# Kernel optimization log

Measured on AMD Instinct MI355X. Metric: run time of the kernel, lower is better.

Reference implementation:

```python
import jax, jax.numpy as jnp
import numpy as np

DIM = 2048
H = 16
HKV = 4
D = DIM // H          # 128 head_dim
ROPE_BASE = 10000.0
TRAIN_SEQ_LEN = 1024
EPS = float(np.finfo(np.float32).eps)  # torch F.rms_norm default eps


def setup_inputs() -> dict:
    key = jax.random.key(0)
    ks = jax.random.split(key, 6)
    B, T = 2, 2048
    return {
        "x": jax.random.normal(ks[0], (B, T, DIM), jnp.float32),
        "q_w": jax.random.normal(ks[1], (DIM, DIM), jnp.float32) * 0.02,
        "k_w": jax.random.normal(ks[2], (HKV * D, DIM), jnp.float32) * 0.02,
        "v_w": jax.random.normal(ks[3], (HKV * D, DIM), jnp.float32) * 0.02,
        "out_w": jax.random.normal(ks[4], (DIM, DIM), jnp.float32) * 0.02,
        "q_gain": jnp.ones((H,), jnp.float32),
    }


def _rope_tables(T, dtype):
    rd = D  # rope_dims == head_dim (rope_dims=0 in module)
    if T > TRAIN_SEQ_LEN:
        scale = T / TRAIN_SEQ_LEN
        base = ROPE_BASE * scale ** (rd / (rd - 2))
    else:
        base = ROPE_BASE
    inv_freq = 1.0 / base ** (np.arange(0, rd, 2, dtype=np.float32) / rd)
    t = np.arange(T, dtype=np.float32)
    freqs = np.outer(t, inv_freq)  # [T, rd/2]
    cos = jnp.asarray(np.cos(freqs), dtype)[None, :, None, :]  # [1,T,1,rd/2]
    sin = jnp.asarray(np.sin(freqs), dtype)[None, :, None, :]
    return cos, sin


def _rms_norm(x):
    var = jnp.mean(jnp.square(x), axis=-1, keepdims=True)
    return x * jax.lax.rsqrt(var + EPS)


def _apply_rotary(x, cos, sin):
    half = x.shape[-1] // 2
    x1, x2 = x[..., :half], x[..., half:]
    return jnp.concatenate((x1 * cos + x2 * sin, -x1 * sin + x2 * cos), axis=-1)


def reference(x, q_w, k_w, v_w, out_w, q_gain):
    B, T, dim = x.shape
    q = (x @ q_w.T).reshape(B, T, H, D)
    k = (x @ k_w.T).reshape(B, T, HKV, D)
    v = (x @ v_w.T).reshape(B, T, HKV, D)
    q = _rms_norm(q)
    k = _rms_norm(k)
    cos, sin = _rope_tables(T, q.dtype)
    q = _apply_rotary(q, cos, sin)
    k = _apply_rotary(k, cos, sin)
    q = q * q_gain[None, None, :, None]
    rep = H // HKV
    k_r = jnp.repeat(k, rep, axis=2)  # [B,T,H,D]
    v_r = jnp.repeat(v, rep, axis=2)
    scores = jnp.einsum('bqhd,bkhd->bhqk', q, k_r) / jnp.sqrt(jnp.asarray(D, q.dtype))
    causal = jnp.tril(jnp.ones((T, T), bool))
    scores = jnp.where(causal[None, None], scores, jnp.asarray(-jnp.inf, scores.dtype))
    p = jax.nn.softmax(scores, axis=-1)
    y = jnp.einsum('bhqk,bkhd->bqhd', p, v_r).reshape(B, T, dim)
    return y @ out_w.T
```

## Files before the change

kernel.cpp:

```cpp
#include <hip/hip_runtime.h>
#include <hip/hip_bf16.h>

typedef __bf16 bf16x8 __attribute__((ext_vector_type(8)));
typedef unsigned short u16x8 __attribute__((ext_vector_type(8)));
typedef float f32x4 __attribute__((ext_vector_type(4)));
typedef __hip_bfloat16 bf16;

#define GLOAD_LDS16(g, l)                                               \
  __builtin_amdgcn_global_load_lds(                                     \
      (__attribute__((address_space(1))) void*)(void*)(g),              \
      (__attribute__((address_space(3))) void*)(void*)(l), 16, 0, 0)

__global__ __launch_bounds__(256) void cvt_all(
    const float4* __restrict__ x,  const float4* __restrict__ qw,
    const float4* __restrict__ kw, const float4* __restrict__ vw,
    const float4* __restrict__ ow,
    ushort4* __restrict__ xb,  ushort4* __restrict__ qwb,
    ushort4* __restrict__ kwb, ushort4* __restrict__ vwb,
    ushort4* __restrict__ owb)
{
  const int i = blockIdx.x * 256 + threadIdx.x;
  const float4* s; ushort4* d; int off;
  if      (i < 2097152) { s = x;  d = xb;  off = i; }
  else if (i < 3145728) { s = qw; d = qwb; off = i - 2097152; }
  else if (i < 3407872) { s = kw; d = kwb; off = i - 3145728; }
  else if (i < 3670016) { s = vw; d = vwb; off = i - 3407872; }
  else                  { s = ow; d = owb; off = i - 3670016; }
  float4 v = s[off];
  bf16 b0 = __float2bfloat16(v.x), b1 = __float2bfloat16(v.y);
  bf16 b2 = __float2bfloat16(v.z), b3 = __float2bfloat16(v.w);
  ushort4 o;
  o.x = *(unsigned short*)&b0; o.y = *(unsigned short*)&b1;
  o.z = *(unsigned short*)&b2; o.w = *(unsigned short*)&b3;
  d[off] = o;
}

__device__ __forceinline__ void store_out(bf16* p, float v)  { *p = __float2bfloat16(v); }
__device__ __forceinline__ void store_out(float* p, float v) { *p = v; }

template <typename OutT>
__device__ __forceinline__ void gemm_tile_body(
    const bf16* __restrict__ A, const bf16* __restrict__ W, OutT* __restrict__ C,
    int bm, int bn, int N, int K, bf16* As, bf16* Ws)
{
  const int tid  = threadIdx.x;
  const int lane = tid & 63;
  const int wave = tid >> 6;
  const int wm = (wave >> 1) * 64;
  const int wn = (wave & 1) * 64;
  const int mfrag = lane & 15;
  const int kfrag = (lane >> 4) * 8;

  f32x4 acc[4][4] = {};

  for (int k0 = 0; k0 < K; k0 += 32) {
#pragma unroll
    for (int r = 0; r < 2; ++r) {
      const int off  = r * 4096 + wave * 1024 + lane * 16;
      const int row  = off >> 6;
      const int colb = off & 63;
      const char* ga = (const char*)A + ((size_t)(bm + row) * K + k0) * 2 + colb;
      GLOAD_LDS16(ga, (char*)As + r * 4096 + wave * 1024);
      const char* gw = (const char*)W + ((size_t)(bn + row) * K + k0) * 2 + colb;
      GLOAD_LDS16(gw, (char*)Ws + r * 4096 + wave * 1024);
    }
    __syncthreads();

    bf16x8 af[4], wf[4];
#pragma unroll
    for (int i = 0; i < 4; ++i)
      af[i] = *(const bf16x8*)(As + (wm + i * 16 + mfrag) * 32 + kfrag);
#pragma unroll
    for (int j = 0; j < 4; ++j)
      wf[j] = *(const bf16x8*)(Ws + (wn + j * 16 + mfrag) * 32 + kfrag);
#pragma unroll
    for (int i = 0; i < 4; ++i)
#pragma unroll
      for (int j = 0; j < 4; ++j)
        acc[i][j] = __builtin_amdgcn_mfma_f32_16x16x32_bf16(af[i], wf[j], acc[i][j], 0, 0, 0);
    __syncthreads();
  }

  const int rq = (lane >> 4) * 4;
#pragma unroll
  for (int i = 0; i < 4; ++i)
#pragma unroll
    for (int j = 0; j < 4; ++j)
#pragma unroll
      for (int r = 0; r < 4; ++r) {
        const int row = bm + wm + i * 16 + rq + r;
        const int col = bn + wn + j * 16 + mfrag;
        store_out(&C[(size_t)row * N + col], acc[i][j][r]);
      }
}

__global__ __launch_bounds__(256) void gemm_bt_f32out(
    const bf16* __restrict__ A, const bf16* __restrict__ W, float* __restrict__ C,
    int N, int K)
{
  __shared__ bf16 As[128 * 32];
  __shared__ bf16 Ws[128 * 32];
  gemm_tile_body<float>(A, W, C, blockIdx.y * 128, blockIdx.x * 128, N, K, As, Ws);
}

__global__ __launch_bounds__(256) void gemm_qkv(
    const bf16* __restrict__ X, const bf16* __restrict__ Wq,
    const bf16* __restrict__ Wk, const bf16* __restrict__ Wv,
    bf16* __restrict__ Qo, bf16* __restrict__ Ko, bf16* __restrict__ Vo, int K)
{
  __shared__ bf16 As[128 * 32];
  __shared__ bf16 Ws[128 * 32];
  const int bx = blockIdx.x;
  const bf16* W; bf16* C; int N, bn;
  if (bx < 16)      { W = Wq; C = Qo; N = 2048; bn = bx * 128; }
  else if (bx < 20) { W = Wk; C = Ko; N = 512;  bn = (bx - 16) * 128; }
  else              { W = Wv; C = Vo; N = 512;  bn = (bx - 20) * 128; }
  gemm_tile_body<bf16>(X, W, C, blockIdx.y * 128, bn, N, K, As, Ws);
}

__device__ __forceinline__ void rope_row(
    bf16* __restrict__ buf, const float* __restrict__ gain,
    int nh, float scale, int row)
{
  const int j = threadIdx.x & 63;
  const int bt = row / nh;
  const int h  = row - bt * nh;
  const int t  = bt & 2047;
  bf16* p = buf + (size_t)bt * (nh * 128) + h * 128;

  float x1 = __bfloat162float(p[j]);
  float x2 = __bfloat162float(p[j + 64]);
  float ss = x1 * x1 + x2 * x2;
#pragma unroll
  for (int off = 32; off > 0; off >>= 1) ss += __shfl_xor(ss, off, 64);
  const float rinv = rsqrtf(ss * (1.0f / 128.0f) + 1.1920928955078125e-07f);
  const float g = gain ? gain[h] : 1.0f;
  const float s = rinv * g * scale;

  const float inv_freq = exp2f(-(float)j * (14.3035853954f / 64.0f));
  const float fr = (float)t * inv_freq;
  const float cs = cosf(fr), sn = sinf(fr);
  p[j]      = __float2bfloat16(s * (x1 * cs + x2 * sn));
  p[j + 64] = __float2bfloat16(s * (x2 * cs - x1 * sn));
}

__global__ __launch_bounds__(256) void postqkv(
    bf16* __restrict__ qb, bf16* __restrict__ kb,
    const unsigned short* __restrict__ vb, unsigned short* __restrict__ vtb,
    const float* __restrict__ gain)
{
  const int bx = blockIdx.x;
  if (bx < 16384) {
    rope_row(qb, gain, 16, 0.08838834764831845f, bx * 4 + (threadIdx.x >> 6));
  } else if (bx < 20480) {
    rope_row(kb, nullptr, 4, 1.0f, (bx - 16384) * 4 + (threadIdx.x >> 6));
  } else {
    const int idx = (bx - 20480) * 256 + threadIdx.x;
    const int t  = idx & 4095;
    const int dc = idx >> 12;
    u16x8 v = *(const u16x8*)(vb + (size_t)t * 512 + dc * 8);
#pragma unroll
    for (int j = 0; j < 8; ++j)
      vtb[(size_t)(dc * 8 + j) * 4096 + t] = v[j];
  }
}

__global__ __launch_bounds__(256) void flash_attn(
    const bf16* __restrict__ Q, const bf16* __restrict__ Kg,
    const bf16* __restrict__ Vtg, bf16* __restrict__ Y)
{
  __shared__ bf16 Ks[2][64 * 128];
  __shared__ bf16 Vs[2][128 * 64];
  __shared__ bf16 Ps[4][16 * 64];

  const int tid = threadIdx.x, lane = tid & 63, w = tid >> 6;
  const int p = blockIdx.x & 15, bh = blockIdx.x >> 4;
  const int h = bh & 15, b = bh >> 4, kvh = h >> 2;
  const int mfrag = lane & 15, quad = lane >> 4;
  const int m7 = mfrag & 7;

  auto stage_k = [&](int kt, int s) {
#pragma unroll
    for (int g = 0; g < 4; ++g) {
      const int o = g * 4096 + w * 1024 + lane * 16;
      const int r = o >> 8, c = (o >> 4) & 15;
      const int cs = (c & 8) | ((c ^ (r & 7)) & 7);
      const bf16* src = Kg + ((size_t)(b * 2048 + kt * 64 + r)) * 512 + kvh * 128 + cs * 8;
      GLOAD_LDS16(src, (char*)&Ks[s][0] + g * 4096 + w * 1024);
    }
  };
  auto stage_v = [&](int kt, int s) {
#pragma unroll
    for (int g = 0; g < 4; ++g) {
      const int o = g * 4096 + w * 1024 + lane * 16;
      const int r = o >> 7, c = (o >> 4) & 7;
      const int cs = (c ^ (r & 7)) & 7;
      const bf16* src = Vtg + ((size_t)(kvh * 128 + r)) * 4096 + b * 2048 + kt * 64 + cs * 8;
      GLOAD_LDS16(src, (char*)&Vs[s][0] + g * 4096 + w * 1024);
    }
  };

  stage_k(0, 0);
  stage_v(0, 0);
  int sb = 0;
  bf16* psw = &Ps[w][0];

  for (int phase = 0; phase < 2; ++phase) {
    const int qt = phase ? p : 31 - p;

    bf16x8 qf[4];
    const bf16* qrow = Q + ((size_t)(b * 2048 + qt * 64 + w * 16 + mfrag)) * 2048 + h * 128;
#pragma unroll
    for (int c = 0; c < 4; ++c) qf[c] = *(const bf16x8*)(qrow + c * 32 + quad * 8);

    f32x4 oacc[8] = {};
    float l_lane[4] = {0.f, 0.f, 0.f, 0.f};
    const int q_base = qt * 64 + w * 16 + quad * 4;

    for (int kt = 0; kt <= qt; ++kt) {
      __syncthreads();
      const bool last = (phase == 1) && (kt == qt);
      if (!last) {
        const int nk = kt < qt ? kt + 1 : 0;
        stage_k(nk, sb ^ 1);
        stage_v(nk, sb ^ 1);
      }

      f32x4 sc[4] = {};
#pragma unroll
      for (int kc = 0; kc < 4; ++kc) {
        const bf16* krow = &Ks[sb][0] + (kc * 16 + mfrag) * 128;
#pragma unroll
        for (int c = 0; c < 4; ++c) {
          const int G = 4 * c + quad;
          const int cs = (G & 8) | ((G ^ m7) & 7);
          bf16x8 kf = *(const bf16x8*)(krow + cs * 8);
          sc[kc] = __builtin_amdgcn_mfma_f32_16x16x32_bf16(qf[c], kf, sc[kc], 0, 0, 0);
        }
      }

      if (kt == qt) {
        const int kcol0 = kt * 64 + mfrag;
#pragma unroll
        for (int kc = 0; kc < 4; ++kc)
#pragma unroll
          for (int r = 0; r < 4; ++r)
            if (kcol0 + kc * 16 > q_base + r) sc[kc][r] = -1e30f;
      }

#pragma unroll
      for (int kc = 0; kc < 4; ++kc)
#pragma unroll
        for (int r = 0; r < 4; ++r) {
          const float pv = __expf(sc[kc][r] - 14.0f);
          l_lane[r] += pv;
          const int q = quad * 4 + r;
          const int slot = ((2 * kc + (mfrag >> 3)) ^ (q & 7)) & 7;
          psw[q * 64 + slot * 8 + m7] = __float2bfloat16(pv);
        }

#pragma unroll
      for (int kh = 0; kh < 2; ++kh) {
        const int Gp = 4 * kh + quad;
        const int sl = (Gp ^ m7) & 7;
        bf16x8 pf = *(const bf16x8*)(psw + mfrag * 64 + sl * 8);
#pragma unroll
        for (int dc = 0; dc < 8; ++dc) {
          bf16x8 vf = *(const bf16x8*)(&Vs[sb][0] + (dc * 16 + mfrag) * 64 + sl * 8);
          oacc[dc] = __builtin_amdgcn_mfma_f32_16x16x32_bf16(pf, vf, oacc[dc], 0, 0, 0);
        }
      }
      sb ^= 1;
    }

#pragma unroll
    for (int r = 0; r < 4; ++r) {
      float l = l_lane[r];
      l += __shfl_xor(l, 1, 64);
      l += __shfl_xor(l, 2, 64);
      l += __shfl_xor(l, 4, 64);
      l += __shfl_xor(l, 8, 64);
      const float linv = 1.0f / l;
      const size_t row = (size_t)(b * 2048 + q_base + r);
#pragma unroll
      for (int dc = 0; dc < 8; ++dc)
        Y[row * 2048 + h * 128 + dc * 16 + mfrag] = __float2bfloat16(oacc[dc][r] * linv);
    }
  }
}

extern "C" void kernel_launch(void* const* d_in, const int* in_sizes, int n_in,
                              void* d_out, int out_size, void* d_ws, size_t ws_size,
                              hipStream_t stream)
{
  const float* x      = (const float*)d_in[0];
  const float* q_w    = (const float*)d_in[1];
  const float* k_w    = (const float*)d_in[2];
  const float* v_w    = (const float*)d_in[3];
  const float* o_w    = (const float*)d_in[4];
  const float* q_gain = (const float*)d_in[5];
  float* out = (float*)d_out;

  char* ws = (char*)d_ws;
  bf16* xb  = (bf16*)(ws);
  bf16* yb  = (bf16*)(ws);
  bf16* qwb = (bf16*)(ws + (16u << 20));
  bf16* vtb = (bf16*)(ws + (16u << 20));
  bf16* owb = (bf16*)(ws + (24u << 20));
  bf16* kwb = (bf16*)(ws + (32u << 20));
  bf16* vwb = (bf16*)(ws + (34u << 20));
  bf16* qb  = (bf16*)(ws + (36u << 20));
  bf16* kb  = (bf16*)(ws + (52u << 20));
  bf16* vb  = (bf16*)(ws + (56u << 20));

  const dim3 blk(256);
  cvt_all<<<dim3(18432), blk, 0, stream>>>(
      (const float4*)x, (const float4*)q_w, (const float4*)k_w,
      (const float4*)v_w, (const float4*)o_w,
      (ushort4*)xb, (ushort4*)qwb, (ushort4*)kwb, (ushort4*)vwb, (ushort4*)owb);

  gemm_qkv<<<dim3(24, 32), blk, 0, stream>>>(xb, qwb, kwb, vwb, qb, kb, vb, 2048);

  postqkv<<<dim3(21504), blk, 0, stream>>>(
      qb, kb, (const unsigned short*)vb, (unsigned short*)vtb, q_gain);

  flash_attn<<<dim3(512), blk, 0, stream>>>(qb, kb, vtb, yb);

  gemm_bt_f32out<<<dim3(16, 32), blk, 0, stream>>>(yb, owb, out, 2048, 2048);
}
```

Measured before the change: 322.6 us.

## Replace GEMMs with 256x256 double-buffered, swizzled, 8-wave pipelined MFMA kernels

Both the QKV projection and output projection GEMMs move from a 128x128 tile with K-step 32 and single-buffered LDS to a 256x256 tile with K-step 64, 512 threads, double-buffered LDS, and an XOR-swizzled layout meant to avoid bank conflicts. Global-to-LDS loads for the next A tile and the B tile two steps ahead are issued in phases interleaved with MFMA work, using explicit vmcnt waits and setprio. The goal is to hide memory latency and raise arithmetic intensity per block. The cost is 128KB of LDS per block, and grids of only 192 and 128 blocks, which may underfill the GPU's CUs.

```diff
diff --git a/kernel.cpp b/kernel.cpp
--- a/kernel.cpp
+++ b/kernel.cpp
@@ -38,84 +38,135 @@
 __device__ __forceinline__ void store_out(bf16* p, float v)  { *p = __float2bfloat16(v); }
 __device__ __forceinline__ void store_out(float* p, float v) { *p = v; }
 
-template <typename OutT>
-__device__ __forceinline__ void gemm_tile_body(
-    const bf16* __restrict__ A, const bf16* __restrict__ W, OutT* __restrict__ C,
-    int bm, int bn, int N, int K, bf16* As, bf16* Ws)
-{
-  const int tid  = threadIdx.x;
-  const int lane = tid & 63;
-  const int wave = tid >> 6;
-  const int wm = (wave >> 1) * 64;
-  const int wn = (wave & 1) * 64;
+template <typename OutT, int K>
+__device__ __forceinline__ void gemm256_body(
+    const bf16* __restrict__ Ag, const bf16* __restrict__ Wg, OutT* __restrict__ C,
+    int bm, int bn, int N, bf16* As0, bf16* As1, bf16* Bs0, bf16* Bs1)
+{
+  constexpr int NT = K / 64;
+  const int tid   = threadIdx.x;
+  const int lane  = tid & 63;
+  const int w     = tid >> 6;
+  const int wr    = w >> 2;
+  const int wc    = w & 3;
   const int mfrag = lane & 15;
-  const int kfrag = (lane >> 4) * 8;
-
-  f32x4 acc[4][4] = {};
-
-  for (int k0 = 0; k0 < K; k0 += 32) {
-#pragma unroll
-    for (int r = 0; r < 2; ++r) {
-      const int off  = r * 4096 + wave * 1024 + lane * 16;
-      const int row  = off >> 6;
-      const int colb = off & 63;
-      const char* ga = (const char*)A + ((size_t)(bm + row) * K + k0) * 2 + colb;
-      GLOAD_LDS16(ga, (char*)As + r * 4096 + wave * 1024);
-      const char* gw = (const char*)W + ((size_t)(bn + row) * K + k0) * 2 + colb;
-      GLOAD_LDS16(gw, (char*)Ws + r * 4096 + wave * 1024);
-    }
-    __syncthreads();
-
-    bf16x8 af[4], wf[4];
-#pragma unroll
-    for (int i = 0; i < 4; ++i)
-      af[i] = *(const bf16x8*)(As + (wm + i * 16 + mfrag) * 32 + kfrag);
+  const int quad  = lane >> 4;
+  const int m7x16 = (mfrag & 7) << 4;
+
+  auto stage_half = [&](const bf16* __restrict__ G, int grow0, int k0, bf16* dsthalf) {
+#pragma unroll
+    for (int l = 0; l < 2; ++l) {
+      const int o    = l * 8192 + tid * 16;
+      const int row  = o >> 7;
+      const int slot = ((o >> 4) & 7) ^ (row & 7);
+      const bf16* src = G + (size_t)(grow0 + row) * K + k0 + slot * 8;
+      GLOAD_LDS16(src, (char*)dsthalf + l * 8192 + w * 1024);
+    }
+  };
+
+  stage_half(Ag, bm,       0, As0);
+  stage_half(Ag, bm + 128, 0, As0 + 8192);
+  stage_half(Wg, bn,       0, Bs0);
+  stage_half(Wg, bn + 128, 0, Bs0 + 8192);
+  if (NT > 1) {
+    stage_half(Wg, bn,       64, Bs1);
+    stage_half(Wg, bn + 128, 64, Bs1 + 8192);
+    asm volatile("s_waitcnt vmcnt(4)" ::: "memory");
+  } else {
+    asm volatile("s_waitcnt vmcnt(0)" ::: "memory");
+  }
+  __builtin_amdgcn_s_barrier();
+
+  f32x4 acc[8][4] = {};
+
+  for (int t = 0; t < NT; ++t) {
+    const char* Ab = (const char*)((t & 1) ? As1 : As0);
+    const char* Bb = (const char*)((t & 1) ? Bs1 : Bs0);
+    bf16* Asn  = (t & 1) ? As0 : As1;
+    bf16* Bsn2 = (t & 1) ? Bs1 : Bs0;
+
+    bf16x8 bfr[4][2];
+#pragma unroll
+    for (int ph = 0; ph < 4; ++ph) {
+      if (ph == 0) {
+#pragma unroll
+        for (int j = 0; j < 4; ++j) {
+          const int rn = wc * 64 + j * 16 + mfrag;
+#pragma unroll
+          for (int kh = 0; kh < 2; ++kh)
+            bfr[j][kh] = *(const bf16x8*)(Bb + ((rn * 128 + kh * 64 + quad * 16) ^ m7x16));
+        }
+      }
+      bf16x8 afr[2][2];
+#pragma unroll
+      for (int r = 0; r < 2; ++r) {
+        const int ra = wr * 128 + (ph * 2 + r) * 16 + mfrag;
+#pragma unroll
+        for (int kh = 0; kh < 2; ++kh)
+          afr[r][kh] = *(const bf16x8*)(Ab + ((ra * 128 + kh * 64 + quad * 16) ^ m7x16));
+      }
+
+      if (ph == 0 && t + 1 < NT) stage_half(Ag, bm,       (t + 1) * 64, Asn);
+      if (ph == 1 && t + 1 < NT) stage_half(Ag, bm + 128, (t + 1) * 64, Asn + 8192);
+      if (ph == 2 && t + 2 < NT) stage_half(Wg, bn,       (t + 2) * 64, Bsn2);
+      if (ph == 3 && t + 2 < NT) stage_half(Wg, bn + 128, (t + 2) * 64, Bsn2 + 8192);
+
+      __builtin_amdgcn_s_barrier();
+      asm volatile("s_waitcnt lgkmcnt(0)" ::: "memory");
+      __builtin_amdgcn_s_setprio(1);
+#pragma unroll
+      for (int r = 0; r < 2; ++r)
+#pragma unroll
+        for (int j = 0; j < 4; ++j)
+#pragma unroll
+          for (int kh = 0; kh < 2; ++kh)
+            acc[ph * 2 + r][j] = __builtin_amdgcn_mfma_f32_16x16x32_bf16(
+                afr[r][kh], bfr[j][kh], acc[ph * 2 + r][j], 0, 0, 0);
+      __builtin_amdgcn_s_setprio(0);
+      if (ph == 3) {
+        if (t < NT - 2) asm volatile("s_waitcnt vmcnt(4)" ::: "memory");
+        else            asm volatile("s_waitcnt vmcnt(0)" ::: "memory");
+      }
+      __builtin_amdgcn_s_barrier();
+    }
+  }
+
+  const int rq = quad * 4;
+#pragma unroll
+  for (int i = 0; i < 8; ++i)
 #pragma unroll
     for (int j = 0; j < 4; ++j)
-      wf[j] = *(const bf16x8*)(Ws + (wn + j * 16 + mfrag) * 32 + kfrag);
-#pragma unroll
-    for (int i = 0; i < 4; ++i)
-#pragma unroll
-      for (int j = 0; j < 4; ++j)
-        acc[i][j] = __builtin_amdgcn_mfma_f32_16x16x32_bf16(af[i], wf[j], acc[i][j], 0, 0, 0);
-    __syncthreads();
-  }
-
-  const int rq = (lane >> 4) * 4;
-#pragma unroll
-  for (int i = 0; i < 4; ++i)
-#pragma unroll
-    for (int j = 0; j < 4; ++j)
 #pragma unroll
       for (int r = 0; r < 4; ++r) {
-        const int row = bm + wm + i * 16 + rq + r;
-        const int col = bn + wn + j * 16 + mfrag;
+        const int row = bm + wr * 128 + i * 16 + rq + r;
+        const int col = bn + wc * 64 + j * 16 + mfrag;
         store_out(&C[(size_t)row * N + col], acc[i][j][r]);
       }
 }
 
-__global__ __launch_bounds__(256) void gemm_bt_f32out(
-    const bf16* __restrict__ A, const bf16* __restrict__ W, float* __restrict__ C,
-    int N, int K)
-{
-  __shared__ bf16 As[128 * 32];
-  __shared__ bf16 Ws[128 * 32];
-  gemm_tile_body<float>(A, W, C, blockIdx.y * 128, blockIdx.x * 128, N, K, As, Ws);
-}
-
-__global__ __launch_bounds__(256) void gemm_qkv(
-    const bf16* __restrict__ X, const bf16* __restrict__ Wq,
+__global__ __launch_bounds__(512, 2) void gemm_qkv256(
+    const bf16* __restrict__ X,  const bf16* __restrict__ Wq,
     const bf16* __restrict__ Wk, const bf16* __restrict__ Wv,
-    bf16* __restrict__ Qo, bf16* __restrict__ Ko, bf16* __restrict__ Vo, int K)
-{
-  __shared__ bf16 As[128 * 32];
-  __shared__ bf16 Ws[128 * 32];
+    bf16* __restrict__ Qo, bf16* __restrict__ Ko, bf16* __restrict__ Vo)
+{
+  __shared__ alignas(16) bf16 As[2][16384];
+  __shared__ alignas(16) bf16 Bs[2][16384];
   const int bx = blockIdx.x;
   const bf16* W; bf16* C; int N, bn;
-  if (bx < 16)      { W = Wq; C = Qo; N = 2048; bn = bx * 128; }
-  else if (bx < 20) { W = Wk; C = Ko; N = 512;  bn = (bx - 16) * 128; }
-  else              { W = Wv; C = Vo; N = 512;  bn = (bx - 20) * 128; }
-  gemm_tile_body<bf16>(X, W, C, blockIdx.y * 128, bn, N, K, As, Ws);
+  if (bx < 8)       { W = Wq; C = Qo; N = 2048; bn = bx * 256; }
+  else if (bx < 10) { W = Wk; C = Ko; N = 512;  bn = (bx - 8) * 256; }
+  else              { W = Wv; C = Vo; N = 512;  bn = (bx - 10) * 256; }
+  gemm256_body<bf16, 2048>(X, W, C, blockIdx.y * 256, bn, N,
+                           As[0], As[1], Bs[0], Bs[1]);
+}
+
+__global__ __launch_bounds__(512, 2) void gemm_out256(
+    const bf16* __restrict__ A, const bf16* __restrict__ W, float* __restrict__ C)
+{
+  __shared__ alignas(16) bf16 As[2][16384];
+  __shared__ alignas(16) bf16 Bs[2][16384];
+  gemm256_body<float, 2048>(A, W, C, blockIdx.y * 256, blockIdx.x * 256, 2048,
+                            As[0], As[1], Bs[0], Bs[1]);
 }
 
 __device__ __forceinline__ void rope_row(
@@ -313,18 +364,17 @@
   bf16* kb  = (bf16*)(ws + (52u << 20));
   bf16* vb  = (bf16*)(ws + (56u << 20));
 
-  const dim3 blk(256);
-  cvt_all<<<dim3(18432), blk, 0, stream>>>(
+  cvt_all<<<dim3(18432), dim3(256), 0, stream>>>(
       (const float4*)x, (const float4*)q_w, (const float4*)k_w,
       (const float4*)v_w, (const float4*)o_w,
       (ushort4*)xb, (ushort4*)qwb, (ushort4*)kwb, (ushort4*)vwb, (ushort4*)owb);
 
-  gemm_qkv<<<dim3(24, 32), blk, 0, stream>>>(xb, qwb, kwb, vwb, qb, kb, vb, 2048);
-
-  postqkv<<<dim3(21504), blk, 0, stream>>>(
+  gemm_qkv256<<<dim3(12, 16), dim3(512), 0, stream>>>(xb, qwb, kwb, vwb, qb, kb, vb);
+
+  postqkv<<<dim3(21504), dim3(256), 0, stream>>>(
       qb, kb, (const unsigned short*)vb, (unsigned short*)vtb, q_gain);
 
-  flash_attn<<<dim3(512), blk, 0, stream>>>(qb, kb, vtb, yb);
-
-  gemm_bt_f32out<<<dim3(16, 32), blk, 0, stream>>>(yb, owb, out, 2048, 2048);
-}
+  flash_attn<<<dim3(512), dim3(256), 0, stream>>>(qb, kb, vtb, yb);
+
+  gemm_out256<<<dim3(8, 16), dim3(512), 0, stream>>>(yb, owb, out);
+}
```

After: 315.5 us. -2.2%, faster.
